# Optimization experiments

Measured on AMD Instinct MI355X. Metric: run time of the kernel, lower is better.

## Reference

```python
import jax, jax.numpy as jnp
import numpy as np

T, SEQ, IN, H, L, NC = 64, 128, 256, 512, 2, 10


def _xavier(key, shape):
    fan_out, fan_in = shape[0], shape[1]
    a = jnp.sqrt(6.0 / (fan_in + fan_out)).astype(jnp.float32)
    return jax.random.uniform(key, shape, jnp.float32, -a, a)


def setup_inputs() -> dict:
    key = jax.random.key(0)
    ks = jax.random.split(key, 16)
    inp = {"x": jax.random.normal(ks[0], (T, SEQ, IN), jnp.float32)}
    # LSTM layer 0 (input IN), layer 1 (input H). PyTorch gate order: i, f, g, o
    inp["w_ih0"] = _xavier(ks[1], (4 * H, IN))
    inp["w_hh0"] = _xavier(ks[2], (4 * H, H))
    inp["b_ih0"] = jnp.zeros((4 * H,), jnp.float32)
    inp["b_hh0"] = jnp.zeros((4 * H,), jnp.float32)
    inp["w_ih1"] = _xavier(ks[3], (4 * H, H))
    inp["w_hh1"] = _xavier(ks[4], (4 * H, H))
    inp["b_ih1"] = jnp.zeros((4 * H,), jnp.float32)
    inp["b_hh1"] = jnp.zeros((4 * H,), jnp.float32)
    # out_linear: Linear(SEQ*H, H) -> ReLU -> Linear(H, NC)
    inp["w1"] = _xavier(ks[5], (H, SEQ * H))
    inp["b1"] = jnp.zeros((H,), jnp.float32)
    inp["w2"] = _xavier(ks[6], (NC, H))
    inp["b2"] = jnp.zeros((NC,), jnp.float32)
    return inp


def _lstm_layer(x, w_ih, w_hh, b_ih, b_hh):
    # x: [T, B, I]; returns hidden sequence [T, B, H]
    B = x.shape[1]
    Hh = w_hh.shape[1]
    # precompute input-to-gate contributions for all timesteps
    xg = jnp.einsum('tbi,gi->tbg', x, w_ih) + b_ih  # [T, B, 4H]

    def step(carry, xg_t):
        h, c = carry
        g = xg_t + h @ w_hh.T + b_hh  # [B, 4H]
        i, f, gg, o = jnp.split(g, 4, axis=-1)
        i = jax.nn.sigmoid(i)
        f = jax.nn.sigmoid(f)
        gg = jnp.tanh(gg)
        o = jax.nn.sigmoid(o)
        c = f * c + i * gg
        h = o * jnp.tanh(c)
        return (h, c), h

    init = (jnp.zeros((B, Hh), x.dtype), jnp.zeros((B, Hh), x.dtype))
    _, ys = jax.lax.scan(step, init, xg)
    return ys


def reference(x, w_ih0, w_hh0, b_ih0, b_hh0, w_ih1, w_hh1, b_ih1, b_hh1, w1, b1, w2, b2):
    out = _lstm_layer(x, w_ih0, w_hh0, b_ih0, b_hh0)
    out = _lstm_layer(out, w_ih1, w_hh1, b_ih1, b_hh1)  # [T, SEQ, H]
    # dropout p=0.0 -> identity
    flat = out.reshape(out.shape[0], -1)  # [T, SEQ*H] (batched version of per-i loop)
    hmid = jax.nn.relu(flat @ w1.T + b1)
    return hmid @ w2.T + b2  # [T, NC]
```

## Files before the change

### kernel.cpp

```cpp
#include <hip/hip_runtime.h>

#define TT 64
#define BB 128
#define IND 256
#define HH 512
#define GG 2048
#define NCC 10
#define KFLAT 65536
#define HP2 520
#define SP 36

typedef __attribute__((ext_vector_type(8))) short bf16x8;
typedef __attribute__((ext_vector_type(4))) float floatx4;

__device__ __forceinline__ unsigned short f2bf(float x) {
    unsigned u = __builtin_bit_cast(unsigned, x);
    u += 0x7fffu + ((u >> 16) & 1u);
    return (unsigned short)(u >> 16);
}
__device__ __forceinline__ float bf2f(unsigned short h) {
    unsigned u = ((unsigned)h) << 16;
    return __builtin_bit_cast(float, u);
}
__device__ __forceinline__ float pk2f(unsigned u) {
    float hi = __builtin_bit_cast(float, u & 0xffff0000u);
    float lo = __builtin_bit_cast(float, u << 16);
    return hi + lo;
}

__global__ __launch_bounds__(256) void pack_split_kernel(
    const float* __restrict__ src, unsigned* __restrict__ dst, int n)
{
    for (int i = blockIdx.x * 256 + threadIdx.x; i < n; i += gridDim.x * 256) {
        float f = src[i];
        unsigned short hb = f2bf(f);
        unsigned short lb = f2bf(f - bf2f(hb));
        dst[i] = ((unsigned)hb << 16) | lb;
    }
}

__global__ __launch_bounds__(256) void gemm_pk_mfma(
    const unsigned* __restrict__ A, const unsigned* __restrict__ W,
    const float* __restrict__ b0, const float* __restrict__ b1,
    float* __restrict__ C, int K, int N)
{
    __shared__ short Ahi[128][SP], Alo[128][SP], Whi[128][SP], Wlo[128][SP];

    const int tid  = threadIdx.x;
    const int lane = tid & 63;
    const int wv   = tid >> 6;
    const int wm   = (wv & 1) * 64;
    const int wn   = (wv >> 1) * 64;
    const int l15  = lane & 15;
    const int quad = lane >> 4;
    const int m0   = blockIdx.x * 128;
    const int n0   = blockIdx.y * 128;

    floatx4 acc[4][4];
    #pragma unroll
    for (int i = 0; i < 4; ++i)
        #pragma unroll
        for (int j = 0; j < 4; ++j)
            acc[i][j] = (floatx4){0.f, 0.f, 0.f, 0.f};

    for (int kc = 0; kc < K; kc += 32) {
        #pragma unroll
        for (int it = 0; it < 4; ++it) {
            const int lin = it * 256 + tid;
            const int row = lin >> 3;
            const int c4  = (lin & 7) * 4;
            uint4 va = *(const uint4*)&A[(size_t)(m0 + row) * K + kc + c4];
            uint2 ah, al;
            ah.x = (va.x >> 16) | (va.y & 0xffff0000u);
            ah.y = (va.z >> 16) | (va.w & 0xffff0000u);
            al.x = (va.x & 0xffffu) | (va.y << 16);
            al.y = (va.z & 0xffffu) | (va.w << 16);
            *(uint2*)&Ahi[row][c4] = ah;
            *(uint2*)&Alo[row][c4] = al;
            uint4 vw = *(const uint4*)&W[(size_t)(n0 + row) * K + kc + c4];
            uint2 wh, wl;
            wh.x = (vw.x >> 16) | (vw.y & 0xffff0000u);
            wh.y = (vw.z >> 16) | (vw.w & 0xffff0000u);
            wl.x = (vw.x & 0xffffu) | (vw.y << 16);
            wl.y = (vw.z & 0xffffu) | (vw.w << 16);
            *(uint2*)&Whi[row][c4] = wh;
            *(uint2*)&Wlo[row][c4] = wl;
        }
        __syncthreads();

        bf16x8 afh[4], afl[4], bfh[4], bfl[4];
        #pragma unroll
        for (int i = 0; i < 4; ++i) {
            afh[i] = *(const bf16x8*)&Ahi[wm + i * 16 + l15][quad * 8];
            afl[i] = *(const bf16x8*)&Alo[wm + i * 16 + l15][quad * 8];
            bfh[i] = *(const bf16x8*)&Whi[wn + i * 16 + l15][quad * 8];
            bfl[i] = *(const bf16x8*)&Wlo[wn + i * 16 + l15][quad * 8];
        }
        #pragma unroll
        for (int i = 0; i < 4; ++i)
            #pragma unroll
            for (int j = 0; j < 4; ++j) {
                acc[i][j] = __builtin_amdgcn_mfma_f32_16x16x32_bf16(afh[i], bfh[j], acc[i][j], 0, 0, 0);
                acc[i][j] = __builtin_amdgcn_mfma_f32_16x16x32_bf16(afh[i], bfl[j], acc[i][j], 0, 0, 0);
                acc[i][j] = __builtin_amdgcn_mfma_f32_16x16x32_bf16(afl[i], bfh[j], acc[i][j], 0, 0, 0);
            }
        __syncthreads();
    }

    #pragma unroll
    for (int i = 0; i < 4; ++i) {
        #pragma unroll
        for (int j = 0; j < 4; ++j) {
            const int n = n0 + wn + j * 16 + l15;
            const float bias = b0[n] + b1[n];
            #pragma unroll
            for (int r = 0; r < 4; ++r) {
                const int m = m0 + wm + i * 16 + quad * 4 + r;
                C[(size_t)m * N + n] = acc[i][j][r] + bias;
            }
        }
    }
}

__device__ __forceinline__ unsigned stage8_atomic(
    const unsigned long long* __restrict__ src, int bb, int kk, unsigned exp,
    short (*Hs_hi)[HP2], short (*Hs_lo)[HP2])
{
    unsigned long long q0 = __hip_atomic_load(src + 0, __ATOMIC_RELAXED, __HIP_MEMORY_SCOPE_AGENT);
    unsigned long long q1 = __hip_atomic_load(src + 1, __ATOMIC_RELAXED, __HIP_MEMORY_SCOPE_AGENT);
    unsigned long long q2 = __hip_atomic_load(src + 2, __ATOMIC_RELAXED, __HIP_MEMORY_SCOPE_AGENT);
    unsigned long long q3 = __hip_atomic_load(src + 3, __ATOMIC_RELAXED, __HIP_MEMORY_SCOPE_AGENT);
    unsigned c0 = (unsigned)q0, c1 = (unsigned)(q0 >> 32);
    unsigned c2 = (unsigned)q1, c3 = (unsigned)(q1 >> 32);
    unsigned c4 = (unsigned)q2, c5 = (unsigned)(q2 >> 32);
    unsigned c6 = (unsigned)q3, c7 = (unsigned)(q3 >> 32);
    unsigned bad = ((c0 ^ exp) | (c1 ^ exp) | (c2 ^ exp) | (c3 ^ exp)
                  | (c4 ^ exp) | (c5 ^ exp) | (c6 ^ exp) | (c7 ^ exp)) & 0xFu;
    uint4 hiv, lov;
    hiv.x = (c0 >> 16) | (c1 & 0xffff0000u);
    hiv.y = (c2 >> 16) | (c3 & 0xffff0000u);
    hiv.z = (c4 >> 16) | (c5 & 0xffff0000u);
    hiv.w = (c6 >> 16) | (c7 & 0xffff0000u);
    lov.x = (c0 & 0xFFF0u) | ((c1 & 0xFFF0u) << 16);
    lov.y = (c2 & 0xFFF0u) | ((c3 & 0xFFF0u) << 16);
    lov.z = (c4 & 0xFFF0u) | ((c5 & 0xFFF0u) << 16);
    lov.w = (c6 & 0xFFF0u) | ((c7 & 0xFFF0u) << 16);
    *(uint4*)&Hs_hi[bb][kk] = hiv;
    *(uint4*)&Hs_lo[bb][kk] = lov;
    return bad;
}

__device__ __forceinline__ unsigned stage8_plain(
    const unsigned* __restrict__ src, int bb, int kk, unsigned exp,
    short (*Hs_hi)[HP2], short (*Hs_lo)[HP2])
{
    const uint4 v0 = *(const uint4*)(src);
    const uint4 v1 = *(const uint4*)(src + 4);
    unsigned bad = ((v0.x ^ exp) | (v0.y ^ exp) | (v0.z ^ exp) | (v0.w ^ exp)
                  | (v1.x ^ exp) | (v1.y ^ exp) | (v1.z ^ exp) | (v1.w ^ exp)) & 0xFu;
    uint4 hiv, lov;
    hiv.x = (v0.x >> 16) | (v0.y & 0xffff0000u);
    hiv.y = (v0.z >> 16) | (v0.w & 0xffff0000u);
    hiv.z = (v1.x >> 16) | (v1.y & 0xffff0000u);
    hiv.w = (v1.z >> 16) | (v1.w & 0xffff0000u);
    lov.x = (v0.x & 0xFFF0u) | ((v0.y & 0xFFF0u) << 16);
    lov.y = (v0.z & 0xFFF0u) | ((v0.w & 0xFFF0u) << 16);
    lov.z = (v1.x & 0xFFF0u) | ((v1.y & 0xFFF0u) << 16);
    lov.w = (v1.z & 0xFFF0u) | ((v1.w & 0xFFF0u) << 16);
    *(uint4*)&Hs_hi[bb][kk] = hiv;
    *(uint4*)&Hs_lo[bb][kk] = lov;
    return bad;
}

__device__ __forceinline__ void stage_tile(
    const unsigned* __restrict__ base, unsigned exp, int tid,
    short (*Hs_hi)[HP2], short (*Hs_lo)[HP2])
{
    unsigned miss = 0;
    #pragma unroll
    for (int p = 0; p < 8; ++p) {
        const int idx = p * 2048 + tid * 8;
        unsigned bad = stage8_plain(base + idx, idx >> 9, idx & 511,
                                    exp, Hs_hi, Hs_lo);
        miss |= (bad ? 1u : 0u) << p;
    }
    while (miss) {
        #pragma unroll
        for (int p = 0; p < 8; ++p) {
            if (miss & (1u << p)) {
                const int idx = p * 2048 + tid * 8;
                if (!stage8_atomic((const unsigned long long*)(base + idx),
                                   idx >> 9, idx & 511, exp, Hs_hi, Hs_lo))
                    miss &= ~(1u << p);
            }
        }
    }
}

__device__ __forceinline__ void spin_flag(const unsigned* p) {
    while (__hip_atomic_load(p, __ATOMIC_RELAXED, __HIP_MEMORY_SCOPE_AGENT) == 0u) { }
}

__global__ __launch_bounds__(256, 1) void lstm_fused(
    const float* __restrict__ xg,
    const float* __restrict__ w_hh0,
    const float* __restrict__ w_ih1,
    const float* __restrict__ w_hh1,
    const float* __restrict__ b_ih1, const float* __restrict__ b_hh1,
    unsigned* __restrict__ hpack0,
    unsigned* __restrict__ hpack1,
    unsigned* __restrict__ flags)
{
    __shared__ short Ra_hi[32][HP2], Ra_lo[32][HP2];
    __shared__ short Xa_hi[32][HP2], Xa_lo[32][HP2];
    __shared__ float Gs[64][33];

    const int tid  = threadIdx.x;
    const int lane = tid & 63;
    const int wv   = tid >> 6;
    const bool isB = blockIdx.x >= 128;
    const int blk  = blockIdx.x & 127;
    const int bt   = blk & 3;
    const int jsl  = blk >> 2;
    const int j0   = jsl * 16;
    const int l15  = lane & 15;
    const int quad = lane >> 4;

    bf16x8 wa_hi[16], wa_lo[16], wx_hi[16], wx_lo[16];
    {
        const float* wsrc = isB ? w_hh1 : w_hh0;
        const float* wrow = wsrc + (size_t)(wv * HH + j0 + l15) * HH + quad * 8;
        #pragma unroll
        for (int kc = 0; kc < 16; ++kc) {
            float f[8];
            *(float4*)&f[0] = *(const float4*)&wrow[kc * 32];
            *(float4*)&f[4] = *(const float4*)&wrow[kc * 32 + 4];
            bf16x8 vh, vl;
            #pragma unroll
            for (int j = 0; j < 8; ++j) {
                unsigned short hb = f2bf(f[j]);
                vh[j] = (short)hb;
                vl[j] = (short)f2bf(f[j] - bf2f(hb));
            }
            wa_hi[kc] = vh; wa_lo[kc] = vl;
        }
        if (isB) {
            const float* xrow = w_ih1 + (size_t)(wv * HH + j0 + l15) * HH + quad * 8;
            #pragma unroll
            for (int kc = 0; kc < 16; ++kc) {
                float f[8];
                *(float4*)&f[0] = *(const float4*)&xrow[kc * 32];
                *(float4*)&f[4] = *(const float4*)&xrow[kc * 32 + 4];
                bf16x8 vh, vl;
                #pragma unroll
                for (int j = 0; j < 8; ++j) {
                    unsigned short hb = f2bf(f[j]);
                    vh[j] = (short)hb;
                    vl[j] = (short)f2bf(f[j] - bf2f(hb));
                }
                wx_hi[kc] = vh; wx_lo[kc] = vl;
            }
        }
    }

    const int j_u = tid & 15;
    const int bu  = tid >> 4;
    float bias_i = 0.f, bias_f = 0.f, bias_g = 0.f, bias_o = 0.f;
    if (isB) {
        bias_i = b_ih1[j0 + j_u]            + b_hh1[j0 + j_u];
        bias_f = b_ih1[HH + j0 + j_u]       + b_hh1[HH + j0 + j_u];
        bias_g = b_ih1[2 * HH + j0 + j_u]   + b_hh1[2 * HH + j0 + j_u];
        bias_o = b_ih1[3 * HH + j0 + j_u]   + b_hh1[3 * HH + j0 + j_u];
    }

    unsigned* hp_rec = isB ? hpack1 : hpack0;
    const int layerBase = isB ? 65 : 0;
    float c0 = 0.f, c1 = 0.f;

    for (int t = 0; t < TT; ++t) {
        const unsigned* rec_base = hp_rec + (size_t)t * (BB * HH) + (size_t)bt * 32 * HH;
        const unsigned* inp_base = hpack0 + (size_t)(t + 1) * (BB * HH) + (size_t)bt * 32 * HH;
        const unsigned expR = (unsigned)t % 9u;
        const unsigned expX = (unsigned)(t + 1) % 9u;
        const unsigned* fR = flags + ((layerBase + t) * 4 + bt) * 32;
        const unsigned* fX = flags + ((t + 1) * 4 + bt) * 32;

        floatx4 a0 = {0.f,0.f,0.f,0.f}, a1 = {0.f,0.f,0.f,0.f};
        float xgv[2][4];

        if (isB) {
            if (wv == 0 && lane < 32) spin_flag(fX + lane);
            __syncthreads();
            stage_tile(inp_base, expX, tid, Xa_hi, Xa_lo);
            __syncthreads();
            #pragma unroll
            for (int kc = 0; kc < 16; ++kc) {
                const int off = kc * 32 + quad * 8;
                bf16x8 x0h = *(const bf16x8*)&Xa_hi[l15][off];
                bf16x8 x0l = *(const bf16x8*)&Xa_lo[l15][off];
                bf16x8 x1h = *(const bf16x8*)&Xa_hi[16 + l15][off];
                bf16x8 x1l = *(const bf16x8*)&Xa_lo[16 + l15][off];
                a0 = __builtin_amdgcn_mfma_f32_16x16x32_bf16(wx_hi[kc], x0h, a0, 0, 0, 0);
                a1 = __builtin_amdgcn_mfma_f32_16x16x32_bf16(wx_hi[kc], x1h, a1, 0, 0, 0);
                a0 = __builtin_amdgcn_mfma_f32_16x16x32_bf16(wx_hi[kc], x0l, a0, 0, 0, 0);
                a1 = __builtin_amdgcn_mfma_f32_16x16x32_bf16(wx_hi[kc], x1l, a1, 0, 0, 0);
                a0 = __builtin_amdgcn_mfma_f32_16x16x32_bf16(wx_lo[kc], x0h, a0, 0, 0, 0);
                a1 = __builtin_amdgcn_mfma_f32_16x16x32_bf16(wx_lo[kc], x1h, a1, 0, 0, 0);
            }
            if (wv == 0 && lane < 32 && t > 0 && lane != jsl) spin_flag(fR + lane);
            __syncthreads();
            stage_tile(rec_base, expR, tid, Ra_hi, Ra_lo);
            __syncthreads();
        } else {
            #pragma unroll
            for (int ccell = 0; ccell < 2; ++ccell) {
                const int b = bu + ccell * 16;
                const float* base = xg + (size_t)t * (BB * GG)
                                  + (size_t)(bt * 32 + b) * GG + j0 + j_u;
                xgv[ccell][0] = base[0];
                xgv[ccell][1] = base[HH];
                xgv[ccell][2] = base[2 * HH];
                xgv[ccell][3] = base[3 * HH];
            }
            if (wv == 0 && lane < 32 && t > 0 && lane != jsl) spin_flag(fR + lane);
            __syncthreads();
            stage_tile(rec_base, expR, tid, Ra_hi, Ra_lo);
            __syncthreads();
        }

        #pragma unroll
        for (int kc = 0; kc < 16; ++kc) {
            const int off = kc * 32 + quad * 8;
            bf16x8 r0h = *(const bf16x8*)&Ra_hi[l15][off];
            bf16x8 r0l = *(const bf16x8*)&Ra_lo[l15][off];
            bf16x8 r1h = *(const bf16x8*)&Ra_hi[16 + l15][off];
            bf16x8 r1l = *(const bf16x8*)&Ra_lo[16 + l15][off];
            a0 = __builtin_amdgcn_mfma_f32_16x16x32_bf16(wa_hi[kc], r0h, a0, 0, 0, 0);
            a1 = __builtin_amdgcn_mfma_f32_16x16x32_bf16(wa_hi[kc], r1h, a1, 0, 0, 0);
            a0 = __builtin_amdgcn_mfma_f32_16x16x32_bf16(wa_hi[kc], r0l, a0, 0, 0, 0);
            a1 = __builtin_amdgcn_mfma_f32_16x16x32_bf16(wa_hi[kc], r1l, a1, 0, 0, 0);
            a0 = __builtin_amdgcn_mfma_f32_16x16x32_bf16(wa_lo[kc], r0h, a0, 0, 0, 0);
            a1 = __builtin_amdgcn_mfma_f32_16x16x32_bf16(wa_lo[kc], r1h, a1, 0, 0, 0);
        }

        #pragma unroll
        for (int r = 0; r < 4; ++r) {
            Gs[wv * 16 + quad * 4 + r][l15]      = a0[r];
            Gs[wv * 16 + quad * 4 + r][16 + l15] = a1[r];
        }
        __syncthreads();

        const unsigned tag = (unsigned)(t + 1) % 9u;
        #pragma unroll
        for (int ccell = 0; ccell < 2; ++ccell) {
            const int b = bu + ccell * 16;
            float gi = Gs[j_u][b],      gf = Gs[16 + j_u][b];
            float gg = Gs[32 + j_u][b], go = Gs[48 + j_u][b];
            if (isB) { gi += bias_i; gf += bias_f; gg += bias_g; go += bias_o; }
            else     { gi += xgv[ccell][0]; gf += xgv[ccell][1];
                       gg += xgv[ccell][2]; go += xgv[ccell][3]; }
            const float si = 1.f / (1.f + __expf(-gi));
            const float sf = 1.f / (1.f + __expf(-gf));
            const float tg = 2.f / (1.f + __expf(-2.f * gg)) - 1.f;
            const float so = 1.f / (1.f + __expf(-go));
            float& cr = ccell ? c1 : c0;
            cr = sf * cr + si * tg;
            const float th = 2.f / (1.f + __expf(-2.f * cr)) - 1.f;
            const float hval = so * th;
            const unsigned short hb = f2bf(hval);
            const unsigned short lb = f2bf(hval - bf2f(hb));
            const unsigned pk = ((unsigned)hb << 16) | ((unsigned)lb & 0xFFF0u) | tag;
            __hip_atomic_store(
                &hp_rec[(size_t)(t + 1) * (BB * HH) + (size_t)(bt * 32 + b) * HH + j0 + j_u],
                pk, __ATOMIC_RELAXED, __HIP_MEMORY_SCOPE_AGENT);
        }
        __syncthreads();

        if (tid == 0)
            __hip_atomic_store(
                flags + ((layerBase + (t + 1)) * 4 + bt) * 32 + jsl,
                1u, __ATOMIC_RELAXED, __HIP_MEMORY_SCOPE_AGENT);
    }
}

__global__ __launch_bounds__(256) void cls_partial_kernel(
    const unsigned* __restrict__ A, const float* __restrict__ W,
    float* __restrict__ part)
{
    const int n0 = blockIdx.x * 64;
    const int s  = blockIdx.y;
    const int kbase = s * 2048;
    const int tid = threadIdx.x;
    __shared__ float As[32][68];
    __shared__ float Bs[32][68];
    const int tm = tid >> 4, tn = tid & 15;
    float acc[4][4] = {};

    for (int kt = 0; kt < 2048; kt += 32) {
        #pragma unroll
        for (int q = tid; q < 512; q += 256) {
            const int mm = q >> 3;
            const int kq = q & 7;
            uint4 v = *(const uint4*)&A[(size_t)mm * KFLAT + kbase + kt + kq * 4];
            As[kq*4+0][mm] = pk2f(v.x & 0xFFFFFFF0u); As[kq*4+1][mm] = pk2f(v.y & 0xFFFFFFF0u);
            As[kq*4+2][mm] = pk2f(v.z & 0xFFFFFFF0u); As[kq*4+3][mm] = pk2f(v.w & 0xFFFFFFF0u);
            float4 w = *(const float4*)&W[(size_t)(n0 + mm) * KFLAT + kbase + kt + kq * 4];
            Bs[kq*4+0][mm] = w.x; Bs[kq*4+1][mm] = w.y;
            Bs[kq*4+2][mm] = w.z; Bs[kq*4+3][mm] = w.w;
        }
        __syncthreads();
        #pragma unroll
        for (int k = 0; k < 32; ++k) {
            float4 a = *(const float4*)&As[k][tm * 4];
            float4 b = *(const float4*)&Bs[k][tn * 4];
            acc[0][0] += a.x*b.x; acc[0][1] += a.x*b.y; acc[0][2] += a.x*b.z; acc[0][3] += a.x*b.w;
            acc[1][0] += a.y*b.x; acc[1][1] += a.y*b.y; acc[1][2] += a.y*b.z; acc[1][3] += a.y*b.w;
            acc[2][0] += a.z*b.x; acc[2][1] += a.z*b.y; acc[2][2] += a.z*b.z; acc[2][3] += a.z*b.w;
            acc[3][0] += a.w*b.x; acc[3][1] += a.w*b.y; acc[3][2] += a.w*b.z; acc[3][3] += a.w*b.w;
        }
        __syncthreads();
    }
    #pragma unroll
    for (int i = 0; i < 4; ++i) {
        const int m = tm * 4 + i;
        #pragma unroll
        for (int j = 0; j < 4; ++j) {
            part[((size_t)s * 64 + m) * 512 + n0 + tn * 4 + j] = acc[i][j];
        }
    }
}

__global__ __launch_bounds__(256) void cls_final_kernel(
    const float* __restrict__ part, const float* __restrict__ b1,
    const float* __restrict__ w2, const float* __restrict__ b2,
    float* __restrict__ out)
{
    const int t = blockIdx.x;
    __shared__ float hm[512];
    for (int n = threadIdx.x; n < 512; n += 256) {
        float sacc = b1[n];
        for (int sl = 0; sl < 32; ++sl)
            sacc += part[((size_t)sl * 64 + t) * 512 + n];
        hm[n] = fmaxf(sacc, 0.f);
    }
    __syncthreads();
    if (threadIdx.x < NCC) {
        float sacc = b2[threadIdx.x];
        const float* wr = w2 + (size_t)threadIdx.x * 512;
        for (int n = 0; n < 512; ++n) sacc += hm[n] * wr[n];
        out[t * NCC + threadIdx.x] = sacc;
    }
}

extern "C" void kernel_launch(void* const* d_in, const int* in_sizes, int n_in,
                              void* d_out, int out_size, void* d_ws, size_t ws_size,
                              hipStream_t stream)
{
    const float* x     = (const float*)d_in[0];
    const float* w_ih0 = (const float*)d_in[1];
    const float* w_hh0 = (const float*)d_in[2];
    const float* b_ih0 = (const float*)d_in[3];
    const float* b_hh0 = (const float*)d_in[4];
    const float* w_ih1 = (const float*)d_in[5];
    const float* w_hh1 = (const float*)d_in[6];
    const float* b_ih1 = (const float*)d_in[7];
    const float* b_hh1 = (const float*)d_in[8];
    const float* w1    = (const float*)d_in[9];
    const float* b1    = (const float*)d_in[10];
    const float* w2    = (const float*)d_in[11];
    const float* b2    = (const float*)d_in[12];
    float* out = (float*)d_out;

    float*    ws     = (float*)d_ws;
    float*    xg     = ws;
    unsigned* hpack0 = (unsigned*)(xg + (size_t)8192 * 2048);
    unsigned* hpack1 = hpack0 + (size_t)65 * BB * HH;
    unsigned* xpk    = hpack1;
    unsigned* w0pk   = xpk + (size_t)8192 * IND;
    float*    part   = (float*)(hpack1 + (size_t)65 * BB * HH);
    unsigned* flags  = (unsigned*)part;

    pack_split_kernel<<<1024, 256, 0, stream>>>(x, xpk, 8192 * IND);
    pack_split_kernel<<<512,  256, 0, stream>>>(w_ih0, w0pk, GG * IND);
    hipMemsetAsync(hpack0, 0, (size_t)BB * HH * sizeof(unsigned), stream);
    hipMemsetAsync(flags, 0, (size_t)2 * 65 * 4 * 32 * sizeof(unsigned), stream);

    gemm_pk_mfma<<<dim3(8192 / 128, GG / 128), 256, 0, stream>>>(
        xpk, w0pk, b_ih0, b_hh0, xg, IND, GG);

    hipMemsetAsync(hpack1, 0, (size_t)BB * HH * sizeof(unsigned), stream);

    lstm_fused<<<256, 256, 0, stream>>>(
        xg, w_hh0, w_ih1, w_hh1, b_ih1, b_hh1, hpack0, hpack1, flags);

    cls_partial_kernel<<<dim3(512 / 64, 32), 256, 0, stream>>>(
        hpack1 + (size_t)BB * HH, w1, part);
    cls_final_kernel<<<64, 256, 0, stream>>>(part, b1, w2, b2, out);
}
```

Baseline: 912.5 us.

## Split LSTM recurrent and input projections across separate wave groups

Doubles the fused LSTM block to 512 threads. Waves 0-3 compute the recurrent h·W_hh product, while waves 4-7 compute the layer-1 input projection at the same time, each writing to its own LDS gate buffer that is summed in the cell update. In layer-0 blocks the extra waves only share the staging of the recurrent tile, so each thread loads half as much. Each wave now holds a single weight set in registers, and the flag spin gains an iteration cap that falls back on the tag-checked staging retry; the cost is more threads per block and idle waves in layer-0 blocks during the MFMA phase.

```diff
diff --git a/kernel.cpp b/kernel.cpp
--- a/kernel.cpp
+++ b/kernel.cpp
@@ -172,23 +172,22 @@
     return bad;
 }
 
-__device__ __forceinline__ void stage_tile(
-    const unsigned* __restrict__ base, unsigned exp, int tid,
+__device__ __forceinline__ void stage_tile_g(
+    const unsigned* __restrict__ base, unsigned exp,
+    int tstart, int pcount, int pstride,
     short (*Hs_hi)[HP2], short (*Hs_lo)[HP2])
 {
     unsigned miss = 0;
-    #pragma unroll
-    for (int p = 0; p < 8; ++p) {
-        const int idx = p * 2048 + tid * 8;
+    for (int p = 0; p < pcount; ++p) {
+        const int idx = p * pstride + tstart;
         unsigned bad = stage8_plain(base + idx, idx >> 9, idx & 511,
                                     exp, Hs_hi, Hs_lo);
         miss |= (bad ? 1u : 0u) << p;
     }
     while (miss) {
-        #pragma unroll
-        for (int p = 0; p < 8; ++p) {
+        for (int p = 0; p < pcount; ++p) {
             if (miss & (1u << p)) {
-                const int idx = p * 2048 + tid * 8;
+                const int idx = p * pstride + tstart;
                 if (!stage8_atomic((const unsigned long long*)(base + idx),
                                    idx >> 9, idx & 511, exp, Hs_hi, Hs_lo))
                     miss &= ~(1u << p);
@@ -198,10 +197,13 @@
 }
 
 __device__ __forceinline__ void spin_flag(const unsigned* p) {
-    while (__hip_atomic_load(p, __ATOMIC_RELAXED, __HIP_MEMORY_SCOPE_AGENT) == 0u) { }
-}
-
-__global__ __launch_bounds__(256, 1) void lstm_fused(
+    int n = 0;
+    while (__hip_atomic_load(p, __ATOMIC_RELAXED, __HIP_MEMORY_SCOPE_AGENT) == 0u) {
+        if (++n > 65536) break;
+    }
+}
+
+__global__ __launch_bounds__(512, 2) void lstm_fused(
     const float* __restrict__ xg,
     const float* __restrict__ w_hh0,
     const float* __restrict__ w_ih1,
@@ -213,11 +215,14 @@
 {
     __shared__ short Ra_hi[32][HP2], Ra_lo[32][HP2];
     __shared__ short Xa_hi[32][HP2], Xa_lo[32][HP2];
-    __shared__ float Gs[64][33];
+    __shared__ float GsR[64][33];
+    __shared__ float GsX[64][33];
 
     const int tid  = threadIdx.x;
     const int lane = tid & 63;
     const int wv   = tid >> 6;
+    const bool isR = wv < 4;
+    const int gate = wv & 3;
     const bool isB = blockIdx.x >= 128;
     const int blk  = blockIdx.x & 127;
     const int bt   = blk & 3;
@@ -225,32 +230,18 @@
     const int j0   = jsl * 16;
     const int l15  = lane & 15;
     const int quad = lane >> 4;
-
-    bf16x8 wa_hi[16], wa_lo[16], wx_hi[16], wx_lo[16];
+    const int tid_x = tid - 256;
+
+    bf16x8 wf_hi[16], wf_lo[16];
     {
-        const float* wsrc = isB ? w_hh1 : w_hh0;
-        const float* wrow = wsrc + (size_t)(wv * HH + j0 + l15) * HH + quad * 8;
-        #pragma unroll
-        for (int kc = 0; kc < 16; ++kc) {
-            float f[8];
-            *(float4*)&f[0] = *(const float4*)&wrow[kc * 32];
-            *(float4*)&f[4] = *(const float4*)&wrow[kc * 32 + 4];
-            bf16x8 vh, vl;
-            #pragma unroll
-            for (int j = 0; j < 8; ++j) {
-                unsigned short hb = f2bf(f[j]);
-                vh[j] = (short)hb;
-                vl[j] = (short)f2bf(f[j] - bf2f(hb));
-            }
-            wa_hi[kc] = vh; wa_lo[kc] = vl;
-        }
-        if (isB) {
-            const float* xrow = w_ih1 + (size_t)(wv * HH + j0 + l15) * HH + quad * 8;
+        const float* wsrc = isR ? (isB ? w_hh1 : w_hh0) : w_ih1;
+        if (isR || isB) {
+            const float* wrow = wsrc + (size_t)(gate * HH + j0 + l15) * HH + quad * 8;
             #pragma unroll
             for (int kc = 0; kc < 16; ++kc) {
                 float f[8];
-                *(float4*)&f[0] = *(const float4*)&xrow[kc * 32];
-                *(float4*)&f[4] = *(const float4*)&xrow[kc * 32 + 4];
+                *(float4*)&f[0] = *(const float4*)&wrow[kc * 32];
+                *(float4*)&f[4] = *(const float4*)&wrow[kc * 32 + 4];
                 bf16x8 vh, vl;
                 #pragma unroll
                 for (int j = 0; j < 8; ++j) {
@@ -258,20 +249,24 @@
                     vh[j] = (short)hb;
                     vl[j] = (short)f2bf(f[j] - bf2f(hb));
                 }
-                wx_hi[kc] = vh; wx_lo[kc] = vl;
+                wf_hi[kc] = vh; wf_lo[kc] = vl;
             }
         }
     }
 
     const int j_u = tid & 15;
-    const int bu  = tid >> 4;
+    const int bu  = (tid >> 4) & 15;
     float bias_i = 0.f, bias_f = 0.f, bias_g = 0.f, bias_o = 0.f;
-    if (isB) {
+    if (isB && isR) {
         bias_i = b_ih1[j0 + j_u]            + b_hh1[j0 + j_u];
         bias_f = b_ih1[HH + j0 + j_u]       + b_hh1[HH + j0 + j_u];
         bias_g = b_ih1[2 * HH + j0 + j_u]   + b_hh1[2 * HH + j0 + j_u];
         bias_o = b_ih1[3 * HH + j0 + j_u]   + b_hh1[3 * HH + j0 + j_u];
     }
+
+    for (int i = tid; i < 64 * 33; i += 512)
+        ((float*)GsX)[i] = 0.f;
+    __syncthreads();
 
     unsigned* hp_rec = isB ? hpack1 : hpack0;
     const int layerBase = isB ? 65 : 0;
@@ -285,33 +280,8 @@
         const unsigned* fR = flags + ((layerBase + t) * 4 + bt) * 32;
         const unsigned* fX = flags + ((t + 1) * 4 + bt) * 32;
 
-        floatx4 a0 = {0.f,0.f,0.f,0.f}, a1 = {0.f,0.f,0.f,0.f};
         float xgv[2][4];
-
-        if (isB) {
-            if (wv == 0 && lane < 32) spin_flag(fX + lane);
-            __syncthreads();
-            stage_tile(inp_base, expX, tid, Xa_hi, Xa_lo);
-            __syncthreads();
-            #pragma unroll
-            for (int kc = 0; kc < 16; ++kc) {
-                const int off = kc * 32 + quad * 8;
-                bf16x8 x0h = *(const bf16x8*)&Xa_hi[l15][off];
-                bf16x8 x0l = *(const bf16x8*)&Xa_lo[l15][off];
-                bf16x8 x1h = *(const bf16x8*)&Xa_hi[16 + l15][off];
-                bf16x8 x1l = *(const bf16x8*)&Xa_lo[16 + l15][off];
-                a0 = __builtin_amdgcn_mfma_f32_16x16x32_bf16(wx_hi[kc], x0h, a0, 0, 0, 0);
-                a1 = __builtin_amdgcn_mfma_f32_16x16x32_bf16(wx_hi[kc], x1h, a1, 0, 0, 0);
-                a0 = __builtin_amdgcn_mfma_f32_16x16x32_bf16(wx_hi[kc], x0l, a0, 0, 0, 0);
-                a1 = __builtin_amdgcn_mfma_f32_16x16x32_bf16(wx_hi[kc], x1l, a1, 0, 0, 0);
-                a0 = __builtin_amdgcn_mfma_f32_16x16x32_bf16(wx_lo[kc], x0h, a0, 0, 0, 0);
-                a1 = __builtin_amdgcn_mfma_f32_16x16x32_bf16(wx_lo[kc], x1h, a1, 0, 0, 0);
-            }
-            if (wv == 0 && lane < 32 && t > 0 && lane != jsl) spin_flag(fR + lane);
-            __syncthreads();
-            stage_tile(rec_base, expR, tid, Ra_hi, Ra_lo);
-            __syncthreads();
-        } else {
+        if (!isB && isR) {
             #pragma unroll
             for (int ccell = 0; ccell < 2; ++ccell) {
                 const int b = bu + ccell * 16;
@@ -322,57 +292,92 @@
                 xgv[ccell][2] = base[2 * HH];
                 xgv[ccell][3] = base[3 * HH];
             }
-            if (wv == 0 && lane < 32 && t > 0 && lane != jsl) spin_flag(fR + lane);
-            __syncthreads();
-            stage_tile(rec_base, expR, tid, Ra_hi, Ra_lo);
-            __syncthreads();
-        }
-
-        #pragma unroll
-        for (int kc = 0; kc < 16; ++kc) {
-            const int off = kc * 32 + quad * 8;
-            bf16x8 r0h = *(const bf16x8*)&Ra_hi[l15][off];
-            bf16x8 r0l = *(const bf16x8*)&Ra_lo[l15][off];
-            bf16x8 r1h = *(const bf16x8*)&Ra_hi[16 + l15][off];
-            bf16x8 r1l = *(const bf16x8*)&Ra_lo[16 + l15][off];
-            a0 = __builtin_amdgcn_mfma_f32_16x16x32_bf16(wa_hi[kc], r0h, a0, 0, 0, 0);
-            a1 = __builtin_amdgcn_mfma_f32_16x16x32_bf16(wa_hi[kc], r1h, a1, 0, 0, 0);
-            a0 = __builtin_amdgcn_mfma_f32_16x16x32_bf16(wa_hi[kc], r0l, a0, 0, 0, 0);
-            a1 = __builtin_amdgcn_mfma_f32_16x16x32_bf16(wa_hi[kc], r1l, a1, 0, 0, 0);
-            a0 = __builtin_amdgcn_mfma_f32_16x16x32_bf16(wa_lo[kc], r0h, a0, 0, 0, 0);
-            a1 = __builtin_amdgcn_mfma_f32_16x16x32_bf16(wa_lo[kc], r1h, a1, 0, 0, 0);
-        }
-
-        #pragma unroll
-        for (int r = 0; r < 4; ++r) {
-            Gs[wv * 16 + quad * 4 + r][l15]      = a0[r];
-            Gs[wv * 16 + quad * 4 + r][16 + l15] = a1[r];
-        }
-        __syncthreads();
-
-        const unsigned tag = (unsigned)(t + 1) % 9u;
-        #pragma unroll
-        for (int ccell = 0; ccell < 2; ++ccell) {
-            const int b = bu + ccell * 16;
-            float gi = Gs[j_u][b],      gf = Gs[16 + j_u][b];
-            float gg = Gs[32 + j_u][b], go = Gs[48 + j_u][b];
-            if (isB) { gi += bias_i; gf += bias_f; gg += bias_g; go += bias_o; }
-            else     { gi += xgv[ccell][0]; gf += xgv[ccell][1];
-                       gg += xgv[ccell][2]; go += xgv[ccell][3]; }
-            const float si = 1.f / (1.f + __expf(-gi));
-            const float sf = 1.f / (1.f + __expf(-gf));
-            const float tg = 2.f / (1.f + __expf(-2.f * gg)) - 1.f;
-            const float so = 1.f / (1.f + __expf(-go));
-            float& cr = ccell ? c1 : c0;
-            cr = sf * cr + si * tg;
-            const float th = 2.f / (1.f + __expf(-2.f * cr)) - 1.f;
-            const float hval = so * th;
-            const unsigned short hb = f2bf(hval);
-            const unsigned short lb = f2bf(hval - bf2f(hb));
-            const unsigned pk = ((unsigned)hb << 16) | ((unsigned)lb & 0xFFF0u) | tag;
-            __hip_atomic_store(
-                &hp_rec[(size_t)(t + 1) * (BB * HH) + (size_t)(bt * 32 + b) * HH + j0 + j_u],
-                pk, __ATOMIC_RELAXED, __HIP_MEMORY_SCOPE_AGENT);
+        }
+
+        if (wv == 0 && lane < 32 && t > 0 && lane != jsl) spin_flag(fR + lane);
+        if (isB && wv == 4 && lane < 32) spin_flag(fX + lane);
+        __syncthreads();
+
+        if (isB) {
+            if (isR) stage_tile_g(rec_base, expR, tid * 8,   8, 2048, Ra_hi, Ra_lo);
+            else     stage_tile_g(inp_base, expX, tid_x * 8, 8, 2048, Xa_hi, Xa_lo);
+        } else {
+            stage_tile_g(rec_base, expR, tid * 8, 4, 4096, Ra_hi, Ra_lo);
+        }
+        __syncthreads();
+
+        if (isR) {
+            floatx4 a0 = {0.f,0.f,0.f,0.f}, a1 = {0.f,0.f,0.f,0.f};
+            #pragma unroll
+            for (int kc = 0; kc < 16; ++kc) {
+                const int off = kc * 32 + quad * 8;
+                bf16x8 r0h = *(const bf16x8*)&Ra_hi[l15][off];
+                bf16x8 r0l = *(const bf16x8*)&Ra_lo[l15][off];
+                bf16x8 r1h = *(const bf16x8*)&Ra_hi[16 + l15][off];
+                bf16x8 r1l = *(const bf16x8*)&Ra_lo[16 + l15][off];
+                a0 = __builtin_amdgcn_mfma_f32_16x16x32_bf16(wf_hi[kc], r0h, a0, 0, 0, 0);
+                a1 = __builtin_amdgcn_mfma_f32_16x16x32_bf16(wf_hi[kc], r1h, a1, 0, 0, 0);
+                a0 = __builtin_amdgcn_mfma_f32_16x16x32_bf16(wf_hi[kc], r0l, a0, 0, 0, 0);
+                a1 = __builtin_amdgcn_mfma_f32_16x16x32_bf16(wf_hi[kc], r1l, a1, 0, 0, 0);
+                a0 = __builtin_amdgcn_mfma_f32_16x16x32_bf16(wf_lo[kc], r0h, a0, 0, 0, 0);
+                a1 = __builtin_amdgcn_mfma_f32_16x16x32_bf16(wf_lo[kc], r1h, a1, 0, 0, 0);
+            }
+            #pragma unroll
+            for (int r = 0; r < 4; ++r) {
+                GsR[gate * 16 + quad * 4 + r][l15]      = a0[r];
+                GsR[gate * 16 + quad * 4 + r][16 + l15] = a1[r];
+            }
+        } else if (isB) {
+            floatx4 a0 = {0.f,0.f,0.f,0.f}, a1 = {0.f,0.f,0.f,0.f};
+            #pragma unroll
+            for (int kc = 0; kc < 16; ++kc) {
+                const int off = kc * 32 + quad * 8;
+                bf16x8 x0h = *(const bf16x8*)&Xa_hi[l15][off];
+                bf16x8 x0l = *(const bf16x8*)&Xa_lo[l15][off];
+                bf16x8 x1h = *(const bf16x8*)&Xa_hi[16 + l15][off];
+                bf16x8 x1l = *(const bf16x8*)&Xa_lo[16 + l15][off];
+                a0 = __builtin_amdgcn_mfma_f32_16x16x32_bf16(wf_hi[kc], x0h, a0, 0, 0, 0);
+                a1 = __builtin_amdgcn_mfma_f32_16x16x32_bf16(wf_hi[kc], x1h, a1, 0, 0, 0);
+                a0 = __builtin_amdgcn_mfma_f32_16x16x32_bf16(wf_hi[kc], x0l, a0, 0, 0, 0);
+                a1 = __builtin_amdgcn_mfma_f32_16x16x32_bf16(wf_hi[kc], x1l, a1, 0, 0, 0);
+                a0 = __builtin_amdgcn_mfma_f32_16x16x32_bf16(wf_lo[kc], x0h, a0, 0, 0, 0);
+                a1 = __builtin_amdgcn_mfma_f32_16x16x32_bf16(wf_lo[kc], x1h, a1, 0, 0, 0);
+            }
+            #pragma unroll
+            for (int r = 0; r < 4; ++r) {
+                GsX[gate * 16 + quad * 4 + r][l15]      = a0[r];
+                GsX[gate * 16 + quad * 4 + r][16 + l15] = a1[r];
+            }
+        }
+        __syncthreads();
+
+        if (isR) {
+            const unsigned tag = (unsigned)(t + 1) % 9u;
+            #pragma unroll
+            for (int ccell = 0; ccell < 2; ++ccell) {
+                const int b = bu + ccell * 16;
+                float gi = GsR[j_u][b]      + GsX[j_u][b];
+                float gf = GsR[16 + j_u][b] + GsX[16 + j_u][b];
+                float gg = GsR[32 + j_u][b] + GsX[32 + j_u][b];
+                float go = GsR[48 + j_u][b] + GsX[48 + j_u][b];
+                if (isB) { gi += bias_i; gf += bias_f; gg += bias_g; go += bias_o; }
+                else     { gi += xgv[ccell][0]; gf += xgv[ccell][1];
+                           gg += xgv[ccell][2]; go += xgv[ccell][3]; }
+                const float si = 1.f / (1.f + __expf(-gi));
+                const float sf = 1.f / (1.f + __expf(-gf));
+                const float tg = 2.f / (1.f + __expf(-2.f * gg)) - 1.f;
+                const float so = 1.f / (1.f + __expf(-go));
+                float& cr = ccell ? c1 : c0;
+                cr = sf * cr + si * tg;
+                const float th = 2.f / (1.f + __expf(-2.f * cr)) - 1.f;
+                const float hval = so * th;
+                const unsigned short hb = f2bf(hval);
+                const unsigned short lb = f2bf(hval - bf2f(hb));
+                const unsigned pk = ((unsigned)hb << 16) | ((unsigned)lb & 0xFFF0u) | tag;
+                __hip_atomic_store(
+                    &hp_rec[(size_t)(t + 1) * (BB * HH) + (size_t)(bt * 32 + b) * HH + j0 + j_u],
+                    pk, __ATOMIC_RELAXED, __HIP_MEMORY_SCOPE_AGENT);
+            }
         }
         __syncthreads();
 
@@ -490,7 +495,7 @@
 
     hipMemsetAsync(hpack1, 0, (size_t)BB * HH * sizeof(unsigned), stream);
 
-    lstm_fused<<<256, 256, 0, stream>>>(
+    lstm_fused<<<256, 512, 0, stream>>>(
         xg, w_hh0, w_ih1, w_hh1, b_ih1, b_hh1, hpack0, hpack1, flags);
 
     cls_partial_kernel<<<dim3(512 / 64, 32), 256, 0, stream>>>(
```

Result: faster. 818.5 us (-10.3%).
